# Kernel optimization log

Hardware: AMD Instinct MI355X
Metric: run time of the kernel (lower is better)

## Reference

```python
import jax, jax.numpy as jnp
import numpy as np

DIM = 1024
NE = 4            # num_experts
MLP = 4           # mlp_ratio
H = 16            # num_heads
HD = DIM // H     # head dim
EXP = 3 * DIM + MLP * DIM   # expand output dim (7*dim)
CIN = DIM + MLP * DIM       # contract input dim (5*dim)


def layer_norm(x, g, b, eps=1e-5):
    m = jnp.mean(x, axis=-1, keepdims=True)
    v = jnp.var(x, axis=-1, keepdims=True)
    return (x - m) * jax.lax.rsqrt(v + eps) * g + b


def setup_inputs() -> dict:
    key = jax.random.key(0)
    ks = jax.random.split(key, 8)
    B, N = 8, 1024
    x = jax.random.normal(ks[0], (B, N, DIM), jnp.float32)
    expert_mask = jax.random.randint(ks[1], (B, N), 0, NE, jnp.int32)
    router_probs = jax.random.uniform(ks[2], (B, N, NE), jnp.float32)
    expand_weight = jax.random.normal(ks[3], (EXP, DIM), jnp.float32) * 0.02
    mlp_bias = jnp.zeros((MLP * DIM,), jnp.float32)
    contract_weight = jax.random.normal(ks[4], (2 * DIM, CIN), jnp.float32) * 0.02
    contract_bias = jnp.zeros((2 * DIM,), jnp.float32)
    norm1_g = jnp.ones((DIM,), jnp.float32)
    norm1_b = jnp.zeros((DIM,), jnp.float32)
    norm2_g = jnp.ones((DIM,), jnp.float32)
    norm2_b = jnp.zeros((DIM,), jnp.float32)
    alpha = jnp.zeros((1,), jnp.float32)
    return dict(x=x, expert_mask=expert_mask, router_probs=router_probs,
                expand_weight=expand_weight, mlp_bias=mlp_bias,
                contract_weight=contract_weight, contract_bias=contract_bias,
                norm1_g=norm1_g, norm1_b=norm1_b, norm2_g=norm2_g, norm2_b=norm2_b,
                alpha=alpha)


def reference(x, expert_mask, router_probs, expand_weight, mlp_bias,
              contract_weight, contract_bias, norm1_g, norm1_b,
              norm2_g, norm2_b, alpha):
    B, N, _ = x.shape
    shift = (NE - 1 - expert_mask).astype(jnp.int32)          # [B,N]
    # nested (matryoshka) active dims per token
    d_in = DIM // jnp.left_shift(1, shift)                    # expand: active input dims
    d_out = (2 * DIM) // jnp.left_shift(1, shift)             # contract: active output dims

    # nested_linear_expand: zero inactive input features, then full GEMM
    in_mask = (jnp.arange(DIM) < d_in[..., None]).astype(x.dtype)
    xn = layer_norm(x, norm1_g, norm1_b) * in_mask
    y = jnp.einsum('bnd,od->bno', xn, expand_weight)          # [B,N,7*dim]

    qkv = y[..., :3 * DIM]
    mlp_hidden = y[..., 3 * DIM:] + mlp_bias

    q = qkv[..., :DIM]
    k = layer_norm(qkv[..., DIM:2 * DIM], norm2_g, norm2_b)
    v = layer_norm(qkv[..., 2 * DIM:], norm2_g, norm2_b)

    qh = q.reshape(B, N, H, HD)
    kh = k.reshape(B, N, H, HD)
    vh = v.reshape(B, N, H, HD)
    scale = HD ** -0.5
    attn = jax.nn.softmax(jnp.einsum('bqhd,bkhd->bhqk', qh, kh) * scale, axis=-1)
    attn_out = jnp.einsum('bhqk,bkhd->bqhd', attn, vh).reshape(B, N, DIM)

    h = jnp.concatenate([attn_out, jax.nn.gelu(mlp_hidden, approximate=False)], axis=-1)
    # nested_linear_contract: full GEMM, zero inactive output features
    z = jnp.einsum('bnc,oc->bno', h, contract_weight) + contract_bias  # [B,N,2*dim]
    z = z * (jnp.arange(2 * DIM) < d_out[..., None]).astype(z.dtype)

    attn_o = z[..., :DIM] + x
    mlp_o = z[..., DIM:]
    expert_probs = jnp.take_along_axis(router_probs, expert_mask[..., None].astype(jnp.int32), axis=-1)  # [B,N,1]
    out = attn_o + (alpha * expert_probs + 1.0) * mlp_o
    return (out, expert_mask, router_probs)
```

## Files before the change

kernel.cpp:

```cpp
#include <hip/hip_runtime.h>
#include <hip/hip_bf16.h>
#include <math.h>

typedef __bf16 bf16_t;
typedef __attribute__((ext_vector_type(8))) __bf16 bf16x8;
typedef __attribute__((ext_vector_type(4))) __bf16 bf16x4;
typedef __attribute__((ext_vector_type(4))) float f32x4;
typedef __attribute__((ext_vector_type(4))) unsigned u32x4;

typedef __attribute__((address_space(1))) unsigned as1u;
typedef __attribute__((address_space(3))) unsigned as3u;

#define MAXT1 68
#define MAXJ2 1056

__device__ __forceinline__ void async_copy16(bf16_t* lds, const bf16_t* g) {
  __builtin_amdgcn_global_load_lds((as1u*)g, (as3u*)lds, 16, 0, 0);
}

__device__ __forceinline__ float gelu_exact(float t) {
  return 0.5f * t * (1.0f + erff(t * 0.70710678118654752f));
}

__device__ __forceinline__ unsigned pack_bf16(float a, float b) {
  unsigned short ha = __builtin_bit_cast(unsigned short, (bf16_t)a);
  unsigned short hb = __builtin_bit_cast(unsigned short, (bf16_t)b);
  return (unsigned)ha | ((unsigned)hb << 16);
}

__global__ __launch_bounds__(256)
void cast_kernel(const float* __restrict__ w, bf16_t* __restrict__ o, int n) {
  int i = (blockIdx.x * 256 + threadIdx.x) * 4;
  if (i < n) {
    float4 v = *(const float4*)(w + i);
    bf16x4 t;
    t[0] = (bf16_t)v.x; t[1] = (bf16_t)v.y; t[2] = (bf16_t)v.z; t[3] = (bf16_t)v.w;
    *(bf16x4*)(o + i) = t;
  }
}

__global__ __launch_bounds__(1024)
void sort_kernel(const int* __restrict__ em, int* __restrict__ perm,
                 int* __restrict__ t1, int* __restrict__ j2) {
  __shared__ int cnt[4], cur[4], tb[5], jb[5];
  const int tid = threadIdx.x;
  const int wave = tid >> 6, lane = tid & 63;
  if (tid < 4) cnt[tid] = 0;
  __syncthreads();
  for (int c = wave; c < 128; c += 16) {
    int e = em[c * 64 + lane];
    unsigned long long m0 = __ballot(e == 0), m1 = __ballot(e == 1);
    unsigned long long m2 = __ballot(e == 2), m3 = __ballot(e == 3);
    if (lane == 0) {
      atomicAdd(&cnt[0], (int)__popcll(m0)); atomicAdd(&cnt[1], (int)__popcll(m1));
      atomicAdd(&cnt[2], (int)__popcll(m2)); atomicAdd(&cnt[3], (int)__popcll(m3));
    }
  }
  __syncthreads();
  if (tid == 0) {
    cur[0] = 0; cur[1] = cnt[0]; cur[2] = cnt[0] + cnt[1]; cur[3] = cnt[0] + cnt[1] + cnt[2];
    tb[0] = 0; jb[0] = 0;
    for (int e = 0; e < 4; ++e) {
      int nt = (cnt[e] + 127) >> 7;
      tb[e + 1] = tb[e] + nt;
      jb[e + 1] = jb[e] + nt * (2 << e);
    }
  }
  __syncthreads();
  for (int c = wave; c < 128; c += 16) {
    int i = c * 64 + lane;
    int e = em[i];
    unsigned long long m0 = __ballot(e == 0), m1 = __ballot(e == 1);
    unsigned long long m2 = __ballot(e == 2), m3 = __ballot(e == 3);
    unsigned long long me = e == 0 ? m0 : e == 1 ? m1 : e == 2 ? m2 : m3;
    int bl = 0;
    if (lane < 4) {
      unsigned long long ml = lane == 0 ? m0 : lane == 1 ? m1 : lane == 2 ? m2 : m3;
      bl = atomicAdd(&cur[lane], (int)__popcll(ml));
    }
    int base = __shfl(bl, e);
    unsigned long long lt = (1ull << lane) - 1ull;
    perm[base + (int)__popcll(me & lt)] = i;
  }
  int offp[5];
  offp[0] = 0;
  #pragma unroll
  for (int e = 0; e < 4; ++e) offp[e + 1] = offp[e] + cnt[e];
  for (int t = tid; t < MAXT1; t += 1024) {
    int e = -1, loc = 0;
    #pragma unroll
    for (int q = 0; q < 4; ++q) if (t >= tb[q] && t < tb[q + 1]) { e = q; loc = t - tb[q]; }
    if (e >= 0) {
      t1[t * 3] = e; t1[t * 3 + 1] = offp[e] + loc * 128;
      t1[t * 3 + 2] = min(128, cnt[e] - loc * 128);
    } else t1[t * 3] = -1;
  }
  for (int j = tid; j < MAXJ2; j += 1024) {
    int e = -1, loc = 0;
    #pragma unroll
    for (int q = 0; q < 4; ++q) if (j >= jb[q] && j < jb[q + 1]) { e = q; loc = j - jb[q]; }
    if (e >= 0) {
      int t = loc >> (1 + e), b = loc & ((2 << e) - 1);
      j2[j * 4] = e; j2[j * 4 + 1] = offp[e] + t * 128;
      j2[j * 4 + 2] = min(128, cnt[e] - t * 128); j2[j * 4 + 3] = b;
    } else j2[j * 4] = -1;
  }
}

__global__ __launch_bounds__(256)
void ln1_kernel(const float* __restrict__ x, const float* __restrict__ gam,
                const float* __restrict__ bet, const int* __restrict__ em,
                bf16_t* __restrict__ xn) {
  const int row = blockIdx.x, tid = threadIdx.x;
  const float4 v = ((const float4*)(x + (size_t)row * 1024))[tid];
  float s = v.x + v.y + v.z + v.w;
  float sq = v.x * v.x + v.y * v.y + v.z * v.z + v.w * v.w;
  #pragma unroll
  for (int off = 1; off < 64; off <<= 1) { s += __shfl_xor(s, off); sq += __shfl_xor(sq, off); }
  __shared__ float red[8];
  const int wave = tid >> 6, lane = tid & 63;
  if (lane == 0) { red[wave] = s; red[4 + wave] = sq; }
  __syncthreads();
  s = red[0] + red[1] + red[2] + red[3];
  sq = red[4] + red[5] + red[6] + red[7];
  const float mean = s * (1.0f / 1024.0f);
  const float var = sq * (1.0f / 1024.0f) - mean * mean;
  const float rstd = rsqrtf(var + 1e-5f);
  const int din = 1024 >> (3 - em[row]);
  const float4 gv = ((const float4*)gam)[tid];
  const float4 bv = ((const float4*)bet)[tid];
  const int c0 = tid * 4;
  float vf[4] = {v.x, v.y, v.z, v.w};
  float gf[4] = {gv.x, gv.y, gv.z, gv.w};
  float bvf[4] = {bv.x, bv.y, bv.z, bv.w};
  bf16x4 o;
  #pragma unroll
  for (int i = 0; i < 4; ++i) {
    float t = (vf[i] - mean) * rstd * gf[i] + bvf[i];
    o[i] = (c0 + i < din) ? (bf16_t)t : (bf16_t)0.0f;
  }
  *(bf16x4*)(xn + (size_t)row * 1024 + c0) = o;
}

__global__ __launch_bounds__(256)
void ln2_kernel(bf16_t* __restrict__ kv, const float* __restrict__ gam,
                const float* __restrict__ bet) {
  const int row = blockIdx.x, tid = threadIdx.x;
  bf16_t* base = kv + (size_t)row * 2048;
  bf16x4 kk = *(const bf16x4*)(base + tid * 4);
  bf16x4 vv = *(const bf16x4*)(base + 1024 + tid * 4);
  float kf[4], vf[4];
  float ks = 0, ksq = 0, vs = 0, vsq = 0;
  #pragma unroll
  for (int i = 0; i < 4; ++i) {
    kf[i] = (float)kk[i]; ks += kf[i]; ksq += kf[i] * kf[i];
    vf[i] = (float)vv[i]; vs += vf[i]; vsq += vf[i] * vf[i];
  }
  #pragma unroll
  for (int off = 1; off < 64; off <<= 1) {
    ks += __shfl_xor(ks, off); ksq += __shfl_xor(ksq, off);
    vs += __shfl_xor(vs, off); vsq += __shfl_xor(vsq, off);
  }
  __shared__ float red[16];
  const int wave = tid >> 6, lane = tid & 63;
  if (lane == 0) { red[wave] = ks; red[4 + wave] = ksq; red[8 + wave] = vs; red[12 + wave] = vsq; }
  __syncthreads();
  ks = red[0] + red[1] + red[2] + red[3];
  ksq = red[4] + red[5] + red[6] + red[7];
  vs = red[8] + red[9] + red[10] + red[11];
  vsq = red[12] + red[13] + red[14] + red[15];
  const float mk = ks * (1.f / 1024.f), mv = vs * (1.f / 1024.f);
  const float rk = rsqrtf(ksq * (1.f / 1024.f) - mk * mk + 1e-5f);
  const float rv = rsqrtf(vsq * (1.f / 1024.f) - mv * mv + 1e-5f);
  const float4 gv = ((const float4*)gam)[tid];
  const float4 bv = ((const float4*)bet)[tid];
  float gf[4] = {gv.x, gv.y, gv.z, gv.w}, bvf[4] = {bv.x, bv.y, bv.z, bv.w};
  bf16x4 ko, vo;
  #pragma unroll
  for (int i = 0; i < 4; ++i) {
    ko[i] = (bf16_t)((kf[i] - mk) * rk * gf[i] + bvf[i]);
    vo[i] = (bf16_t)((vf[i] - mv) * rv * gf[i] + bvf[i]);
  }
  *(bf16x4*)(base + tid * 4) = ko;
  *(bf16x4*)(base + 1024 + tid * 4) = vo;
}

__global__ __launch_bounds__(256)
void vt_kernel(const bf16_t* __restrict__ kv, bf16_t* __restrict__ vT) {
  __shared__ bf16_t t[64][80];
  const int tt = blockIdx.x, head = blockIdx.y;
  const int tid = threadIdx.x;
  const int r8 = tid >> 3, c8 = tid & 7;
  #pragma unroll
  for (int i = 0; i < 2; ++i) {
    const int tok = i * 32 + r8;
    bf16x8 v = *(const bf16x8*)(kv + (size_t)(tt * 64 + tok) * 2048 + 1024 + head * 64 + c8 * 8);
    #pragma unroll
    for (int j = 0; j < 8; ++j) t[c8 * 8 + j][tok] = v[j];
  }
  __syncthreads();
  const int bb = tt >> 4;
  const int tloc = (tt & 15) * 64;
  #pragma unroll
  for (int i = 0; i < 2; ++i) {
    const int d = i * 32 + r8;
    bf16x8 v = *(const bf16x8*)(&t[d][c8 * 8]);
    *(bf16x8*)(vT + (size_t)((bb * 16 + head) * 64 + d) * 1024 + tloc + c8 * 8) = v;
  }
}

template<int EPI>
__global__ __launch_bounds__(256)
void gemm_bt(const bf16_t* __restrict__ A, const bf16_t* __restrict__ W,
             const int* __restrict__ perm, const int* __restrict__ desc,
             const float* __restrict__ bias,
             bf16_t* __restrict__ hb, bf16_t* __restrict__ kvb,
             float* __restrict__ z_attn, bf16_t* __restrict__ z_mlp) {
  constexpr int K = (EPI == 0) ? 1024 : 5120;
  const int* d = desc + blockIdx.x * ((EPI == 0) ? 3 : 4);
  const int e = d[0];
  if (e < 0) return;
  const int nval = d[2];
  const int bn = (EPI == 0) ? blockIdx.y : d[3];
  const int nkt = (EPI == 0) ? (2 << e) : 80;

  __shared__ bf16_t As[128 * 64];
  __shared__ bf16_t Bs[128 * 64];
  __shared__ int prow[128];
  const int tid = threadIdx.x;
  if (tid < 128) prow[tid] = perm[d[1] + min(tid, nval - 1)];
  const int wave = tid >> 6, lane = tid & 63;
  const int l15 = lane & 15, l4 = lane >> 4;
  const int wm = wave >> 1, wn = wave & 1;

  f32x4 acc[4][4] = {};

  const int rbase = tid >> 3;
  const int ss = (tid & 7) ^ (rbase & 7);
  __syncthreads();
  const bf16_t* Ag[4];
  #pragma unroll
  for (int i = 0; i < 4; ++i) Ag[i] = A + (size_t)prow[i * 32 + rbase] * K + ss * 8;
  const bf16_t* Wg = W + (size_t)(bn * 128 + rbase) * K + ss * 8;

  for (int kt = 0; kt < nkt; ++kt) {
    #pragma unroll
    for (int i = 0; i < 4; ++i) {
      async_copy16(As + (i * 256 + wave * 64) * 8, Ag[i] + kt * 64);
      async_copy16(Bs + (i * 256 + wave * 64) * 8, Wg + (size_t)i * 32 * K + kt * 64);
    }
    __syncthreads();
    #pragma unroll
    for (int ks = 0; ks < 2; ++ks) {
      bf16x8 a[4], b[4];
      #pragma unroll
      for (int mi = 0; mi < 4; ++mi) {
        const int r = wm * 64 + mi * 16 + l15;
        const int slot = (ks * 4 + l4) ^ (r & 7);
        a[mi] = *(const bf16x8*)(As + r * 64 + slot * 8);
      }
      #pragma unroll
      for (int ni = 0; ni < 4; ++ni) {
        const int r = wn * 64 + ni * 16 + l15;
        const int slot = (ks * 4 + l4) ^ (r & 7);
        b[ni] = *(const bf16x8*)(Bs + r * 64 + slot * 8);
      }
      #pragma unroll
      for (int mi = 0; mi < 4; ++mi)
        #pragma unroll
        for (int ni = 0; ni < 4; ++ni)
          acc[mi][ni] = __builtin_amdgcn_mfma_f32_16x16x32_bf16(a[mi], b[ni], acc[mi][ni], 0, 0, 0);
    }
    __syncthreads();
  }

  #pragma unroll
  for (int mi = 0; mi < 4; ++mi) {
    #pragma unroll
    for (int ni = 0; ni < 4; ++ni) {
      const int gc = bn * 128 + wn * 64 + ni * 16 + l15;
      #pragma unroll
      for (int r = 0; r < 4; ++r) {
        const int gml = wm * 64 + mi * 16 + l4 * 4 + r;
        if (gml < nval) {
          const size_t token = (size_t)prow[gml];
          const float c = acc[mi][ni][r];
          if (EPI == 0) {
            if (gc < 1024) {
              hb[token * 5120 + gc] = (bf16_t)c;
            } else if (gc < 3072) {
              kvb[token * 2048 + (gc - 1024)] = (bf16_t)c;
            } else {
              const float t = c + bias[gc - 3072];
              hb[token * 5120 + 1024 + (gc - 3072)] = (bf16_t)gelu_exact(t);
            }
          } else {
            const float t = c + bias[gc];
            if (gc < 1024) z_attn[token * 1024 + gc] = t;
            else           z_mlp[token * 1024 + (gc - 1024)] = (bf16_t)t;
          }
        }
      }
    }
  }
}

__global__ __launch_bounds__(256)
void attn_kernel(const bf16_t* __restrict__ kv, const bf16_t* __restrict__ vT,
                 bf16_t* __restrict__ hb) {
  __shared__ bf16_t Kl[64 * 64];
  __shared__ bf16_t Vl[64 * 64];
  const int tid = threadIdx.x;
  const int wave = tid >> 6, lane = tid & 63;
  const int l15 = lane & 15, l4 = lane >> 4;
  const int qt = blockIdx.x, bh = blockIdx.y;
  const int bb = bh >> 4;
  const int tok0 = bb << 10;
  const int d0 = (bh & 15) << 6;

  const int qrow = tok0 + qt * 64 + wave * 16 + l15;
  const bf16x8 bq0 = *(const bf16x8*)(hb + (size_t)qrow * 5120 + d0 + l4 * 8);
  const bf16x8 bq1 = *(const bf16x8*)(hb + (size_t)qrow * 5120 + d0 + 32 + l4 * 8);

  f32x4 o[4] = {};
  float mrun = -1e30f, lrun = 0.f;

  const int krb = tid >> 3;
  const int kss = (tid & 7) ^ (krb & 7);
  const int idx0 = ((2 * (l4 & 1) + 0) * 16 + l15) * 4;
  const int idx1 = ((2 * (l4 & 1) + 1) * 16 + l15) * 4;
  const bool hi = (l4 >> 1) != 0;

  for (int kt = 0; kt < 16; ++kt) {
    const int krow0 = tok0 + kt * 64;
    #pragma unroll
    for (int i = 0; i < 2; ++i) {
      async_copy16(Kl + (i * 256 + wave * 64) * 8,
                   kv + (size_t)(krow0 + i * 32 + krb) * 2048 + d0 + kss * 8);
      async_copy16(Vl + (i * 256 + wave * 64) * 8,
                   vT + (size_t)(bh * 64 + i * 32 + krb) * 1024 + kt * 64 + kss * 8);
    }
    __syncthreads();

    f32x4 s[4] = {};
    #pragma unroll
    for (int ks = 0; ks < 2; ++ks) {
      const bf16x8 bq = ks ? bq1 : bq0;
      #pragma unroll
      for (int kc = 0; kc < 4; ++kc) {
        const int r = kc * 16 + l15;
        const int slot = (ks * 4 + l4) ^ (r & 7);
        bf16x8 ak = *(const bf16x8*)(Kl + r * 64 + slot * 8);
        s[kc] = __builtin_amdgcn_mfma_f32_16x16x32_bf16(ak, bq, s[kc], 0, 0, 0);
      }
    }

    float mx = s[0][0];
    #pragma unroll
    for (int kc = 0; kc < 4; ++kc)
      #pragma unroll
      for (int r = 0; r < 4; ++r) mx = fmaxf(mx, s[kc][r]);
    mx = fmaxf(mx, __shfl_xor(mx, 16));
    mx = fmaxf(mx, __shfl_xor(mx, 32));
    mx *= 0.125f;
    const float mnew = fmaxf(mrun, mx);
    const float corr = __expf(mrun - mnew);
    float ps = 0.f;
    #pragma unroll
    for (int kc = 0; kc < 4; ++kc)
      #pragma unroll
      for (int r = 0; r < 4; ++r) {
        const float p = __expf(s[kc][r] * 0.125f - mnew);
        s[kc][r] = p;
        ps += p;
      }
    ps += __shfl_xor(ps, 16);
    ps += __shfl_xor(ps, 32);
    lrun = lrun * corr + ps;
    mrun = mnew;

    unsigned pd[4][2], bp[4][2][2];
    #pragma unroll
    for (int kc = 0; kc < 4; ++kc) {
      pd[kc][0] = pack_bf16(s[kc][0], s[kc][1]);
      pd[kc][1] = pack_bf16(s[kc][2], s[kc][3]);
    }
    #pragma unroll
    for (int kc = 0; kc < 4; ++kc)
      #pragma unroll
      for (int rp = 0; rp < 2; ++rp) {
        bp[kc][rp][0] = (unsigned)__builtin_amdgcn_ds_bpermute(idx0, (int)pd[kc][rp]);
        bp[kc][rp][1] = (unsigned)__builtin_amdgcn_ds_bpermute(idx1, (int)pd[kc][rp]);
      }
    u32x4 w0, w1;
    w0[0] = hi ? bp[1][0][0] : bp[0][0][0];
    w0[1] = hi ? bp[1][1][0] : bp[0][1][0];
    w0[2] = hi ? bp[1][0][1] : bp[0][0][1];
    w0[3] = hi ? bp[1][1][1] : bp[0][1][1];
    w1[0] = hi ? bp[3][0][0] : bp[2][0][0];
    w1[1] = hi ? bp[3][1][0] : bp[2][1][0];
    w1[2] = hi ? bp[3][0][1] : bp[2][0][1];
    w1[3] = hi ? bp[3][1][1] : bp[2][1][1];
    const bf16x8 pa0 = __builtin_bit_cast(bf16x8, w0);
    const bf16x8 pa1 = __builtin_bit_cast(bf16x8, w1);

    float cq[4];
    #pragma unroll
    for (int r = 0; r < 4; ++r) cq[r] = __shfl(corr, l4 * 4 + r);
    #pragma unroll
    for (int dn = 0; dn < 4; ++dn)
      #pragma unroll
      for (int r = 0; r < 4; ++r) o[dn][r] *= cq[r];

    #pragma unroll
    for (int dn = 0; dn < 4; ++dn) {
      const int r = dn * 16 + l15;
      bf16x8 bv0 = *(const bf16x8*)(Vl + r * 64 + ((l4 ^ (r & 7)) * 8));
      bf16x8 bv1 = *(const bf16x8*)(Vl + r * 64 + (((4 + l4) ^ (r & 7)) * 8));
      o[dn] = __builtin_amdgcn_mfma_f32_16x16x32_bf16(pa0, bv0, o[dn], 0, 0, 0);
      o[dn] = __builtin_amdgcn_mfma_f32_16x16x32_bf16(pa1, bv1, o[dn], 0, 0, 0);
    }
    __syncthreads();
  }

  const float il = 1.0f / lrun;
  float linv[4];
  #pragma unroll
  for (int r = 0; r < 4; ++r) linv[r] = __shfl(il, l4 * 4 + r);
  #pragma unroll
  for (int r = 0; r < 4; ++r) {
    const int gq = tok0 + qt * 64 + wave * 16 + l4 * 4 + r;
    #pragma unroll
    for (int dn = 0; dn < 4; ++dn)
      hb[(size_t)gq * 5120 + d0 + dn * 16 + l15] = (bf16_t)(o[dn][r] * linv[r]);
  }
}

__global__ __launch_bounds__(256)
void final_kernel(const float* __restrict__ z_attn, const bf16_t* __restrict__ z_mlp,
                  const float* __restrict__ x, const int* __restrict__ em,
                  const float* __restrict__ rp, const float* __restrict__ alpha,
                  float* __restrict__ out) {
  const int row = blockIdx.x, tid = threadIdx.x;
  const int e = em[row];
  const int dout = 2048 >> (3 - e);
  const float f = alpha[0] * rp[row * 4 + e] + 1.0f;
  const float4 z0 = ((const float4*)(z_attn + (size_t)row * 1024))[tid];
  const bf16x4 z1 = ((const bf16x4*)(z_mlp + (size_t)row * 1024))[tid];
  const float4 xv = ((const float4*)(x + (size_t)row * 1024))[tid];
  const int c = tid * 4;
  float4 o;
  o.x = ((c + 0) < dout ? z0.x : 0.f) + xv.x + f * ((1024 + c + 0) < dout ? (float)z1[0] : 0.f);
  o.y = ((c + 1) < dout ? z0.y : 0.f) + xv.y + f * ((1024 + c + 1) < dout ? (float)z1[1] : 0.f);
  o.z = ((c + 2) < dout ? z0.z : 0.f) + xv.z + f * ((1024 + c + 2) < dout ? (float)z1[2] : 0.f);
  o.w = ((c + 3) < dout ? z0.w : 0.f) + xv.w + f * ((1024 + c + 3) < dout ? (float)z1[3] : 0.f);
  ((float4*)(out + (size_t)row * 1024))[tid] = o;
  float* out_em = out + 8388608;
  float* out_rp = out_em + 8192;
  if (tid == 0) out_em[row] = (float)e;
  if (tid < 4) out_rp[row * 4 + tid] = rp[row * 4 + tid];
}

extern "C" void kernel_launch(void* const* d_in, const int* in_sizes, int n_in,
                              void* d_out, int out_size, void* d_ws, size_t ws_size,
                              hipStream_t stream) {
  const float* x = (const float*)d_in[0];
  const int* em = (const int*)d_in[1];
  const float* rp = (const float*)d_in[2];
  const float* w_exp = (const float*)d_in[3];
  const float* mlp_bias = (const float*)d_in[4];
  const float* w_con = (const float*)d_in[5];
  const float* c_bias = (const float*)d_in[6];
  const float* n1g = (const float*)d_in[7];
  const float* n1b = (const float*)d_in[8];
  const float* n2g = (const float*)d_in[9];
  const float* n2b = (const float*)d_in[10];
  const float* alpha = (const float*)d_in[11];

  char* ws = (char*)d_ws;
  bf16_t* Wexp  = (bf16_t*)ws;
  bf16_t* xn    = (bf16_t*)(ws + 14680064);
  bf16_t* vT    = (bf16_t*)(ws + 14680064);
  bf16_t* z_mlp = (bf16_t*)(ws + 14680064);
  int*    perm  = (int*)(ws + 31457280);
  int*    t1d   = (int*)(ws + 31457280 + 32768);
  int*    j2d   = (int*)(ws + 31457280 + 34816);
  bf16_t* kvb   = (bf16_t*)(ws + 48234496);
  float*  z_att = (float*)(ws + 48234496);
  bf16_t* Wcon  = (bf16_t*)(ws + 81788928);
  bf16_t* hb    = (bf16_t*)(ws + 102760448);

  sort_kernel<<<1, 1024, 0, stream>>>(em, perm, t1d, j2d);
  cast_kernel<<<7168, 256, 0, stream>>>(w_exp, Wexp, 7340032);
  cast_kernel<<<10240, 256, 0, stream>>>(w_con, Wcon, 10485760);
  ln1_kernel<<<8192, 256, 0, stream>>>(x, n1g, n1b, em, xn);
  gemm_bt<0><<<dim3(MAXT1, 56), 256, 0, stream>>>(xn, Wexp, perm, t1d, mlp_bias,
                                                  hb, kvb, nullptr, nullptr);
  ln2_kernel<<<8192, 256, 0, stream>>>(kvb, n2g, n2b);
  vt_kernel<<<dim3(128, 16), 256, 0, stream>>>(kvb, vT);
  attn_kernel<<<dim3(16, 128), 256, 0, stream>>>(kvb, vT, hb);
  gemm_bt<1><<<MAXJ2, 256, 0, stream>>>(hb, Wcon, perm, j2d, c_bias,
                                        nullptr, nullptr, z_att, z_mlp);
  final_kernel<<<8192, 256, 0, stream>>>(z_att, z_mlp, x, em, rp, alpha, (float*)d_out);
}
```

Before: 426.1 us.

## Stage GEMM epilogues through LDS, shrink contract tile, reorder expand-grid scheduling

The GEMM epilogue now writes accumulators into shared memory and then issues coalesced 16-byte stores per token row, replacing scattered per-element stores. The contract GEMM uses a 64-wide N tile, which doubles its block count, and writes a single bf16 z buffer instead of an fp32 attention half plus a bf16 MLP half. The expand GEMM grid is transposed so column tiles vary fastest, and tiles are ordered with the largest experts first to improve weight reuse and load balance. The trade-offs are lower precision for the attention residual term (bf16 instead of fp32), less A-tile reuse per contract block, and an extra LDS round trip in the epilogue.

After: 439.4 us. +3.1%, slower.

```diff
diff --git a/kernel.cpp b/kernel.cpp
--- a/kernel.cpp
+++ b/kernel.cpp
@@ -12,7 +12,7 @@
 typedef __attribute__((address_space(3))) unsigned as3u;
 
 #define MAXT1 68
-#define MAXJ2 1056
+#define MAXJ2 2112
 
 __device__ __forceinline__ void async_copy16(bf16_t* lds, const bf16_t* g) {
   __builtin_amdgcn_global_load_lds((as1u*)g, (as3u*)lds, 16, 0, 0);
@@ -60,10 +60,13 @@
   if (tid == 0) {
     cur[0] = 0; cur[1] = cnt[0]; cur[2] = cnt[0] + cnt[1]; cur[3] = cnt[0] + cnt[1] + cnt[2];
     tb[0] = 0; jb[0] = 0;
+    for (int i = 0; i < 4; ++i) {
+      int e = 3 - i;
+      tb[i + 1] = tb[i] + ((cnt[e] + 127) >> 7);
+    }
     for (int e = 0; e < 4; ++e) {
       int nt = (cnt[e] + 127) >> 7;
-      tb[e + 1] = tb[e] + nt;
-      jb[e + 1] = jb[e] + nt * (2 << e);
+      jb[e + 1] = jb[e] + nt * (4 << e);
     }
   }
   __syncthreads();
@@ -89,7 +92,7 @@
   for (int t = tid; t < MAXT1; t += 1024) {
     int e = -1, loc = 0;
     #pragma unroll
-    for (int q = 0; q < 4; ++q) if (t >= tb[q] && t < tb[q + 1]) { e = q; loc = t - tb[q]; }
+    for (int i = 0; i < 4; ++i) if (t >= tb[i] && t < tb[i + 1]) { e = 3 - i; loc = t - tb[i]; }
     if (e >= 0) {
       t1[t * 3] = e; t1[t * 3 + 1] = offp[e] + loc * 128;
       t1[t * 3 + 2] = min(128, cnt[e] - loc * 128);
@@ -100,7 +103,7 @@
     #pragma unroll
     for (int q = 0; q < 4; ++q) if (j >= jb[q] && j < jb[q + 1]) { e = q; loc = j - jb[q]; }
     if (e >= 0) {
-      int t = loc >> (1 + e), b = loc & ((2 << e) - 1);
+      int t = loc >> (2 + e), b = loc & ((4 << e) - 1);
       j2[j * 4] = e; j2[j * 4 + 1] = offp[e] + t * 128;
       j2[j * 4 + 2] = min(128, cnt[e] - t * 128); j2[j * 4 + 3] = b;
     } else j2[j * 4] = -1;
@@ -215,25 +218,30 @@
              const int* __restrict__ perm, const int* __restrict__ desc,
              const float* __restrict__ bias,
              bf16_t* __restrict__ hb, bf16_t* __restrict__ kvb,
-             float* __restrict__ z_attn, bf16_t* __restrict__ z_mlp) {
+             bf16_t* __restrict__ z) {
   constexpr int K = (EPI == 0) ? 1024 : 5120;
-  const int* d = desc + blockIdx.x * ((EPI == 0) ? 3 : 4);
+  constexpr int BN = (EPI == 0) ? 128 : 64;
+  constexpr int NI = BN / 32;
+  constexpr int WC = BN / 2;
+  const int* d = desc + ((EPI == 0) ? blockIdx.y * 3 : blockIdx.x * 4);
   const int e = d[0];
   if (e < 0) return;
   const int nval = d[2];
-  const int bn = (EPI == 0) ? blockIdx.y : d[3];
+  const int bn = (EPI == 0) ? blockIdx.x : d[3];
   const int nkt = (EPI == 0) ? (2 << e) : 80;
 
-  __shared__ bf16_t As[128 * 64];
-  __shared__ bf16_t Bs[128 * 64];
+  __shared__ bf16_t SMEM[17408];
   __shared__ int prow[128];
+  bf16_t* As = SMEM;
+  bf16_t* Bs = SMEM + 8192;
+
   const int tid = threadIdx.x;
   if (tid < 128) prow[tid] = perm[d[1] + min(tid, nval - 1)];
   const int wave = tid >> 6, lane = tid & 63;
   const int l15 = lane & 15, l4 = lane >> 4;
   const int wm = wave >> 1, wn = wave & 1;
 
-  f32x4 acc[4][4] = {};
+  f32x4 acc[4][NI] = {};
 
   const int rbase = tid >> 3;
   const int ss = (tid & 7) ^ (rbase & 7);
@@ -241,18 +249,19 @@
   const bf16_t* Ag[4];
   #pragma unroll
   for (int i = 0; i < 4; ++i) Ag[i] = A + (size_t)prow[i * 32 + rbase] * K + ss * 8;
-  const bf16_t* Wg = W + (size_t)(bn * 128 + rbase) * K + ss * 8;
+  const bf16_t* Wg = W + (size_t)(bn * BN + rbase) * K + ss * 8;
 
   for (int kt = 0; kt < nkt; ++kt) {
     #pragma unroll
-    for (int i = 0; i < 4; ++i) {
+    for (int i = 0; i < 4; ++i)
       async_copy16(As + (i * 256 + wave * 64) * 8, Ag[i] + kt * 64);
-      async_copy16(Bs + (i * 256 + wave * 64) * 8, Wg + (size_t)i * 32 * K + kt * 64);
-    }
+    #pragma unroll
+    for (int i = 0; i < NI; ++i)
+      async_copy16(Bs + (i * 256 + wave * 64) * 8, Wg + (size_t)(i * 32) * K + kt * 64);
     __syncthreads();
     #pragma unroll
     for (int ks = 0; ks < 2; ++ks) {
-      bf16x8 a[4], b[4];
+      bf16x8 a[4], b[NI];
       #pragma unroll
       for (int mi = 0; mi < 4; ++mi) {
         const int r = wm * 64 + mi * 16 + l15;
@@ -260,15 +269,15 @@
         a[mi] = *(const bf16x8*)(As + r * 64 + slot * 8);
       }
       #pragma unroll
-      for (int ni = 0; ni < 4; ++ni) {
-        const int r = wn * 64 + ni * 16 + l15;
+      for (int ni = 0; ni < NI; ++ni) {
+        const int r = wn * WC + ni * 16 + l15;
         const int slot = (ks * 4 + l4) ^ (r & 7);
         b[ni] = *(const bf16x8*)(Bs + r * 64 + slot * 8);
       }
       #pragma unroll
       for (int mi = 0; mi < 4; ++mi)
         #pragma unroll
-        for (int ni = 0; ni < 4; ++ni)
+        for (int ni = 0; ni < NI; ++ni)
           acc[mi][ni] = __builtin_amdgcn_mfma_f32_16x16x32_bf16(a[mi], b[ni], acc[mi][ni], 0, 0, 0);
     }
     __syncthreads();
@@ -277,29 +286,48 @@
   #pragma unroll
   for (int mi = 0; mi < 4; ++mi) {
     #pragma unroll
-    for (int ni = 0; ni < 4; ++ni) {
-      const int gc = bn * 128 + wn * 64 + ni * 16 + l15;
+    for (int ni = 0; ni < NI; ++ni) {
+      const int colf = wn * WC + ni * 16 + l15;
       #pragma unroll
       for (int r = 0; r < 4; ++r) {
-        const int gml = wm * 64 + mi * 16 + l4 * 4 + r;
-        if (gml < nval) {
-          const size_t token = (size_t)prow[gml];
-          const float c = acc[mi][ni][r];
-          if (EPI == 0) {
-            if (gc < 1024) {
-              hb[token * 5120 + gc] = (bf16_t)c;
-            } else if (gc < 3072) {
-              kvb[token * 2048 + (gc - 1024)] = (bf16_t)c;
-            } else {
-              const float t = c + bias[gc - 3072];
-              hb[token * 5120 + 1024 + (gc - 3072)] = (bf16_t)gelu_exact(t);
-            }
-          } else {
-            const float t = c + bias[gc];
-            if (gc < 1024) z_attn[token * 1024 + gc] = t;
-            else           z_mlp[token * 1024 + (gc - 1024)] = (bf16_t)t;
-          }
+        const int row = wm * 64 + mi * 16 + l4 * 4 + r;
+        const float c = acc[mi][ni][r];
+        bf16_t v;
+        if (EPI == 0) {
+          const int gc = bn * 128 + colf;
+          v = (gc >= 3072) ? (bf16_t)gelu_exact(c + bias[gc - 3072]) : (bf16_t)c;
+        } else {
+          v = (bf16_t)(c + bias[bn * 64 + colf]);
         }
+        SMEM[row * 136 + colf] = v;
+      }
+    }
+  }
+  __syncthreads();
+  if (EPI == 0) {
+    const int col0 = (tid & 15) * 8;
+    const int gc0 = bn * 128 + col0;
+    #pragma unroll
+    for (int i = 0; i < 8; ++i) {
+      const int row = (tid >> 4) * 8 + i;
+      if (row < nval) {
+        const size_t token = (size_t)prow[row];
+        bf16x8 v = *(const bf16x8*)(SMEM + row * 136 + col0);
+        if (gc0 < 1024)      *(bf16x8*)(hb + token * 5120 + gc0) = v;
+        else if (gc0 < 3072) *(bf16x8*)(kvb + token * 2048 + (gc0 - 1024)) = v;
+        else                 *(bf16x8*)(hb + token * 5120 + 1024 + (gc0 - 3072)) = v;
+      }
+    }
+  } else {
+    const int col0 = (tid & 7) * 8;
+    const int gc0 = bn * 64 + col0;
+    #pragma unroll
+    for (int i = 0; i < 4; ++i) {
+      const int row = (tid >> 3) * 4 + i;
+      if (row < nval) {
+        const size_t token = (size_t)prow[row];
+        bf16x8 v = *(const bf16x8*)(SMEM + row * 136 + col0);
+        *(bf16x8*)(z + token * 2048 + gc0) = v;
       }
     }
   }
@@ -437,23 +465,22 @@
 }
 
 __global__ __launch_bounds__(256)
-void final_kernel(const float* __restrict__ z_attn, const bf16_t* __restrict__ z_mlp,
-                  const float* __restrict__ x, const int* __restrict__ em,
-                  const float* __restrict__ rp, const float* __restrict__ alpha,
-                  float* __restrict__ out) {
+void final_kernel(const bf16_t* __restrict__ z, const float* __restrict__ x,
+                  const int* __restrict__ em, const float* __restrict__ rp,
+                  const float* __restrict__ alpha, float* __restrict__ out) {
   const int row = blockIdx.x, tid = threadIdx.x;
   const int e = em[row];
   const int dout = 2048 >> (3 - e);
   const float f = alpha[0] * rp[row * 4 + e] + 1.0f;
-  const float4 z0 = ((const float4*)(z_attn + (size_t)row * 1024))[tid];
-  const bf16x4 z1 = ((const bf16x4*)(z_mlp + (size_t)row * 1024))[tid];
+  const bf16x4 z0 = ((const bf16x4*)(z + (size_t)row * 2048))[tid];
+  const bf16x4 z1 = ((const bf16x4*)(z + (size_t)row * 2048 + 1024))[tid];
   const float4 xv = ((const float4*)(x + (size_t)row * 1024))[tid];
   const int c = tid * 4;
   float4 o;
-  o.x = ((c + 0) < dout ? z0.x : 0.f) + xv.x + f * ((1024 + c + 0) < dout ? (float)z1[0] : 0.f);
-  o.y = ((c + 1) < dout ? z0.y : 0.f) + xv.y + f * ((1024 + c + 1) < dout ? (float)z1[1] : 0.f);
-  o.z = ((c + 2) < dout ? z0.z : 0.f) + xv.z + f * ((1024 + c + 2) < dout ? (float)z1[2] : 0.f);
-  o.w = ((c + 3) < dout ? z0.w : 0.f) + xv.w + f * ((1024 + c + 3) < dout ? (float)z1[3] : 0.f);
+  o.x = ((c + 0) < dout ? (float)z0[0] : 0.f) + xv.x + f * ((1024 + c + 0) < dout ? (float)z1[0] : 0.f);
+  o.y = ((c + 1) < dout ? (float)z0[1] : 0.f) + xv.y + f * ((1024 + c + 1) < dout ? (float)z1[1] : 0.f);
+  o.z = ((c + 2) < dout ? (float)z0[2] : 0.f) + xv.z + f * ((1024 + c + 2) < dout ? (float)z1[2] : 0.f);
+  o.w = ((c + 3) < dout ? (float)z0[3] : 0.f) + xv.w + f * ((1024 + c + 3) < dout ? (float)z1[3] : 0.f);
   ((float4*)(out + (size_t)row * 1024))[tid] = o;
   float* out_em = out + 8388608;
   float* out_rp = out_em + 8192;
@@ -478,28 +505,27 @@
   const float* alpha = (const float*)d_in[11];
 
   char* ws = (char*)d_ws;
-  bf16_t* Wexp  = (bf16_t*)ws;
-  bf16_t* xn    = (bf16_t*)(ws + 14680064);
-  bf16_t* vT    = (bf16_t*)(ws + 14680064);
-  bf16_t* z_mlp = (bf16_t*)(ws + 14680064);
-  int*    perm  = (int*)(ws + 31457280);
-  int*    t1d   = (int*)(ws + 31457280 + 32768);
-  int*    j2d   = (int*)(ws + 31457280 + 34816);
-  bf16_t* kvb   = (bf16_t*)(ws + 48234496);
-  float*  z_att = (float*)(ws + 48234496);
-  bf16_t* Wcon  = (bf16_t*)(ws + 81788928);
-  bf16_t* hb    = (bf16_t*)(ws + 102760448);
+  bf16_t* Wexp = (bf16_t*)ws;
+  bf16_t* xn   = (bf16_t*)(ws + 14680064);
+  bf16_t* vT   = (bf16_t*)(ws + 14680064);
+  int*    perm = (int*)(ws + 31457280);
+  int*    t1d  = (int*)(ws + 31457280 + 32768);
+  int*    j2d  = (int*)(ws + 31457280 + 34816);
+  bf16_t* kvb  = (bf16_t*)(ws + 48234496);
+  bf16_t* z    = (bf16_t*)(ws + 48234496);
+  bf16_t* Wcon = (bf16_t*)(ws + 81788928);
+  bf16_t* hb   = (bf16_t*)(ws + 102760448);
 
   sort_kernel<<<1, 1024, 0, stream>>>(em, perm, t1d, j2d);
   cast_kernel<<<7168, 256, 0, stream>>>(w_exp, Wexp, 7340032);
   cast_kernel<<<10240, 256, 0, stream>>>(w_con, Wcon, 10485760);
   ln1_kernel<<<8192, 256, 0, stream>>>(x, n1g, n1b, em, xn);
-  gemm_bt<0><<<dim3(MAXT1, 56), 256, 0, stream>>>(xn, Wexp, perm, t1d, mlp_bias,
-                                                  hb, kvb, nullptr, nullptr);
+  gemm_bt<0><<<dim3(56, MAXT1), 256, 0, stream>>>(xn, Wexp, perm, t1d, mlp_bias,
+                                                  hb, kvb, nullptr);
   ln2_kernel<<<8192, 256, 0, stream>>>(kvb, n2g, n2b);
   vt_kernel<<<dim3(128, 16), 256, 0, stream>>>(kvb, vT);
   attn_kernel<<<dim3(16, 128), 256, 0, stream>>>(kvb, vT, hb);
   gemm_bt<1><<<MAXJ2, 256, 0, stream>>>(hb, Wcon, perm, j2d, c_bias,
-                                        nullptr, nullptr, z_att, z_mlp);
-  final_kernel<<<8192, 256, 0, stream>>>(z_att, z_mlp, x, em, rp, alpha, (float*)d_out);
-}
+                                        nullptr, nullptr, z);
+  final_kernel<<<8192, 256, 0, stream>>>(z, x, em, rp, alpha, (float*)d_out);
+}
```
